# Optimization experiments

Hardware: AMD Instinct MI355X
Metric: run time of the kernel (lower is better)

The kernel has to match this reference:

```python
import jax, jax.numpy as jnp
import numpy as np

D_MODEL, D_STATE, D_CONV, EXPAND, L = 512, 16, 4, 2, 2048
D_INNER = EXPAND * D_MODEL


def _dwconv_causal(x, w, b):
    # x: (L, D), w: (D, K), b: (D,). torch Conv1d(groups=D, padding=K-1)[..., :L]
    K = w.shape[1]
    xp = jnp.pad(x, ((K - 1, 0), (0, 0)))
    windows = jnp.stack([xp[k:k + x.shape[0]] for k in range(K)], axis=-1)  # (L, D, K)
    return jnp.einsum('ldk,dk->ld', windows, w) + b


def _ssm_dir(x, inW, inb, cw, cb, xpW, xpb, dtW, dtb, outW, outb, A_log, Dp):
    xz = x @ inW + inb                      # (L, 2*Di)
    x_ssm, z = xz[:, :D_INNER], xz[:, D_INNER:]
    x_ssm = _dwconv_causal(x_ssm, cw, cb)   # (L, Di)
    sp = jax.nn.silu(x_ssm) @ xpW + xpb     # (L, Di + 2*S)
    delta = sp[:, :D_INNER]
    B = sp[:, D_INNER:D_INNER + D_STATE]
    C = sp[:, D_INNER + D_STATE:]
    dt = jax.nn.softplus(delta @ dtW + dtb)  # (L, Di)
    A = -jnp.exp(A_log)                      # (Di, S)
    dA = jnp.exp(dt[:, :, None] * A[None])                      # (L, Di, S)
    dBu = dt[:, :, None] * B[:, None, :] * x_ssm[:, :, None]    # (L, Di, S)

    def step(h, inp):
        a, bu = inp
        h = a * h + bu
        return h, h

    h0 = jnp.zeros((D_INNER, D_STATE), x.dtype)
    _, hs = jax.lax.scan(step, h0, (dA, dBu))   # (L, Di, S)
    y = jnp.einsum('lds,ls->ld', hs, C) + Dp * x_ssm
    return (y * jax.nn.silu(z)) @ outW + outb


def _make_params(key):
    ks = jax.random.split(key, 32)
    i = iter(range(32))
    def w(shape, scale=0.02):
        return (jax.random.normal(ks[next(i)], shape, jnp.float32) * scale)
    p = {}
    for pre in ('fwd_', 'bwd_'):
        p[pre + 'in_W'] = w((D_MODEL, 2 * D_INNER))
        p[pre + 'in_b'] = w((2 * D_INNER,))
        p[pre + 'conv_w'] = w((D_INNER, D_CONV), 0.1)
        p[pre + 'conv_b'] = w((D_INNER,))
        p[pre + 'xp_W'] = w((D_INNER, D_INNER + 2 * D_STATE))
        p[pre + 'xp_b'] = w((D_INNER + 2 * D_STATE,))
        p[pre + 'dt_W'] = w((D_INNER, D_INNER))
        p[pre + 'dt_b'] = w((D_INNER,))
        p[pre + 'out_W'] = w((D_INNER, D_MODEL))
        p[pre + 'out_b'] = w((D_MODEL,))
    p['A_log'] = jax.random.normal(ks[next(i)], (D_INNER, D_STATE), jnp.float32) * 0.5
    p['D_param'] = jnp.ones((D_INNER,), jnp.float32)
    p['fusion_W'] = w((2 * D_MODEL, D_MODEL))
    p['fusion_b'] = w((D_MODEL,))
    return p


def setup_inputs() -> dict:
    key = jax.random.key(0)
    kx, kp = jax.random.split(key)
    inp = {'x': jax.random.normal(kx, (L, D_MODEL), jnp.float32)}
    inp.update(_make_params(kp))
    return inp


def reference(x,
              fwd_in_W, fwd_in_b, fwd_conv_w, fwd_conv_b, fwd_xp_W, fwd_xp_b,
              fwd_dt_W, fwd_dt_b, fwd_out_W, fwd_out_b,
              bwd_in_W, bwd_in_b, bwd_conv_w, bwd_conv_b, bwd_xp_W, bwd_xp_b,
              bwd_dt_W, bwd_dt_b, bwd_out_W, bwd_out_b,
              A_log, D_param, fusion_W, fusion_b):
    out_fwd = _ssm_dir(x, fwd_in_W, fwd_in_b, fwd_conv_w, fwd_conv_b,
                       fwd_xp_W, fwd_xp_b, fwd_dt_W, fwd_dt_b,
                       fwd_out_W, fwd_out_b, A_log, D_param)
    out_bwd = _ssm_dir(x[::-1], bwd_in_W, bwd_in_b, bwd_conv_w, bwd_conv_b,
                       bwd_xp_W, bwd_xp_b, bwd_dt_W, bwd_dt_b,
                       bwd_out_W, bwd_out_b, A_log, D_param)[::-1]
    return jnp.concatenate([out_fwd, out_bwd], axis=-1) @ fusion_W + fusion_b
```

## Files before the change

### kernel.cpp

```cpp
#include <hip/hip_runtime.h>
#include <cmath>

#define L_SEQ 2048
#define DM 512
#define DI 1024
#define DS 16
#define NSP 1056
#define NC 64
#define CL 32

typedef unsigned short ushortT;
typedef unsigned int u32;
typedef __attribute__((ext_vector_type(8))) short short8;
typedef __attribute__((ext_vector_type(4))) float float4_t;
typedef __attribute__((address_space(1))) u32 gu32;
typedef __attribute__((address_space(3))) u32 lu32;

__device__ __forceinline__ float sigm(float x) { return 1.0f / (1.0f + __expf(-x)); }

__device__ __forceinline__ ushortT f2bf(float f) {
    unsigned u = __float_as_uint(f);
    unsigned r = u + 0x7FFFu + ((u >> 16) & 1u);
    return (ushortT)(r >> 16);
}

__device__ __forceinline__ void gl2lds16(const ushortT* g, ushortT* l) {
    __builtin_amdgcn_global_load_lds((gu32*)g, (lu32*)l, 16, 0, 0);
}

__global__ __launch_bounds__(256) void wcvt_k(const float* __restrict__ W,
                                              ushortT* __restrict__ Wt,
                                              int K, int N)
{
    __shared__ ushortT t[32][33];
    int n0 = blockIdx.x * 32, k0 = blockIdx.y * 32;
    int tx = threadIdx.x & 31, ty = threadIdx.x >> 5;
    #pragma unroll
    for (int i = 0; i < 32; i += 8)
        t[ty + i][tx] = f2bf(W[(size_t)(k0 + ty + i) * N + n0 + tx]);
    __syncthreads();
    #pragma unroll
    for (int i = 0; i < 32; i += 8)
        Wt[(size_t)(n0 + ty + i) * K + k0 + tx] = t[tx][ty + i];
}

__global__ __launch_bounds__(256) void xcvt_k(const float* __restrict__ x,
                                              ushortT* __restrict__ xb, int n)
{
    int i = (blockIdx.x * 256 + threadIdx.x) * 4;
    if (i < n) {
        float4_t v = *(const float4_t*)(x + i);
        xb[i + 0] = f2bf(v[0]); xb[i + 1] = f2bf(v[1]);
        xb[i + 2] = f2bf(v[2]); xb[i + 3] = f2bf(v[3]);
    }
}

template<int BM, int BN>
__global__ __launch_bounds__(256, 2) void gemm_bf16(
    const ushortT* __restrict__ A, int lda, long long Astr, int revAmode,
    const ushortT* __restrict__ W, long long Wstr,
    const float* __restrict__ bias0, const float* __restrict__ bias1,
    float* __restrict__ Cf, int ldcf, long long Cfstr,
    ushortT* __restrict__ Cb, int ldcb, long long Cbstr, int Nbmax,
    int revCmode, int M, int N, int K, int epi)
{
    const int dir = blockIdx.z;
    A  += (size_t)dir * Astr;
    W  += (size_t)dir * Wstr;
    if (Cf) Cf += (size_t)dir * Cfstr;
    if (Cb) Cb += (size_t)dir * Cbstr;
    const float* bias = dir ? bias1 : bias0;
    const int revA = (revAmode == 2) ? dir : revAmode;
    const int revC = (revCmode == 2) ? dir : revCmode;

    constexpr int MI = BM / 32;
    constexpr int NI = BN / 32;
    constexpr int CA = BM / 64;
    constexpr int CB = BN / 64;

    __shared__ ushortT As[BM * 32];
    __shared__ ushortT Bs[BN * 32];

    const int tid  = threadIdx.x;
    const int wave = tid >> 6;
    const int lane = tid & 63;
    const int quad = lane >> 4;
    const int r    = lane & 15;
    const int wm   = (wave >> 1) * (BM / 2);
    const int wn   = (wave & 1) * (BN / 2);
    const int bm   = blockIdx.y * BM;
    const int bn   = blockIdx.x * BN;

    const int lrow = lane >> 2;
    const int lk   = (lane & 3) * 8;

    const ushortT* gA[CA];
    ushortT* lA[CA];
    #pragma unroll
    for (int c = 0; c < CA; ++c) {
        int row = bm + c * 64 + wave * 16 + lrow;
        if (revA) row = M - 1 - row;
        gA[c] = A + (size_t)row * lda + lk;
        lA[c] = As + (c * 64 + wave * 16) * 32;
    }
    const ushortT* gB[CB];
    ushortT* lB[CB];
    #pragma unroll
    for (int c = 0; c < CB; ++c) {
        int row = bn + c * 64 + wave * 16 + lrow;
        if (row > N - 1) row = N - 1;
        gB[c] = W + (size_t)row * K + lk;
        lB[c] = Bs + (c * 64 + wave * 16) * 32;
    }

    float4_t acc[MI][NI];
    #pragma unroll
    for (int i = 0; i < MI; ++i)
        #pragma unroll
        for (int j = 0; j < NI; ++j)
            acc[i][j] = (float4_t){0.f, 0.f, 0.f, 0.f};

    for (int k0 = 0; k0 < K; k0 += 32) {
        #pragma unroll
        for (int c = 0; c < CA; ++c) gl2lds16(gA[c] + k0, lA[c]);
        #pragma unroll
        for (int c = 0; c < CB; ++c) gl2lds16(gB[c] + k0, lB[c]);
        __syncthreads();

        short8 af[MI], bf[NI];
        #pragma unroll
        for (int mi = 0; mi < MI; ++mi)
            af[mi] = *(const short8*)&As[(wm + mi * 16 + r) * 32 + quad * 8];
        #pragma unroll
        for (int ni = 0; ni < NI; ++ni)
            bf[ni] = *(const short8*)&Bs[(wn + ni * 16 + r) * 32 + quad * 8];
        #pragma unroll
        for (int mi = 0; mi < MI; ++mi)
            #pragma unroll
            for (int ni = 0; ni < NI; ++ni)
                acc[mi][ni] = __builtin_amdgcn_mfma_f32_16x16x32_bf16(
                    af[mi], bf[ni], acc[mi][ni], 0, 0, 0);
        __syncthreads();
    }

    #pragma unroll
    for (int mi = 0; mi < MI; ++mi) {
        int rowb = bm + wm + mi * 16 + quad * 4;
        #pragma unroll
        for (int ni = 0; ni < NI; ++ni) {
            int gn = bn + wn + ni * 16 + r;
            if (gn < N) {
                float bv = bias[gn];
                #pragma unroll
                for (int j = 0; j < 4; ++j) {
                    int orow = rowb + j;
                    if (revC) orow = M - 1 - orow;
                    float v = acc[mi][ni][j] + bv;
                    if (epi == 1) v = (v > 20.0f) ? v : log1pf(__expf(v));
                    if (Cf) Cf[(size_t)orow * ldcf + gn] = v;
                    if (Cb && gn < Nbmax) Cb[(size_t)orow * ldcb + gn] = f2bf(v);
                }
            }
        }
    }
}

__global__ __launch_bounds__(256) void conv_k(
    const float* __restrict__ XZ, const float* __restrict__ cw,
    const float* __restrict__ cb, float* __restrict__ XC, ushortT* __restrict__ SCb)
{
    int idx = blockIdx.x * 256 + threadIdx.x;
    int d = idx & (DI - 1);
    int l = idx >> 10;
    float w0 = cw[d * 4 + 0], w1 = cw[d * 4 + 1], w2 = cw[d * 4 + 2], w3 = cw[d * 4 + 3];
    float acc = cb[d];
    if (l >= 3) acc += XZ[(size_t)(l - 3) * (2 * DI) + d] * w0;
    if (l >= 2) acc += XZ[(size_t)(l - 2) * (2 * DI) + d] * w1;
    if (l >= 1) acc += XZ[(size_t)(l - 1) * (2 * DI) + d] * w2;
    acc += XZ[(size_t)l * (2 * DI) + d] * w3;
    XC[idx] = acc;
    SCb[idx] = f2bf(acc * sigm(acc));
}

__global__ __launch_bounds__(256) void scanA_k(
    const float* __restrict__ DT, const float* __restrict__ XC,
    const float* __restrict__ SP, const float* __restrict__ Alog,
    float* __restrict__ Pend, float* __restrict__ Hl)
{
    __shared__ float Bsh[CL][DS];
    int dir = blockIdx.z;
    int c = blockIdx.y;
    int d = blockIdx.x * 256 + threadIdx.x;
    DT += (size_t)dir * L_SEQ * DI;
    XC += (size_t)dir * L_SEQ * DI;
    SP += (size_t)dir * L_SEQ * NSP;
    int l0 = c * CL;
    for (int i = threadIdx.x; i < CL * DS; i += 256) {
        int ll = i >> 4, ss = i & 15;
        Bsh[ll][ss] = SP[(size_t)(l0 + ll) * NSP + DI + ss];
    }
    __syncthreads();
    float Ae[DS], h[DS], P[DS];
    #pragma unroll
    for (int s = 0; s < DS; ++s) { Ae[s] = -__expf(Alog[d * DS + s]); h[s] = 0.f; P[s] = 1.f; }
    for (int t = 0; t < CL; ++t) {
        int l = l0 + t;
        float dt = DT[(size_t)l * DI + d];
        float xv = XC[(size_t)l * DI + d];
        float dtx = dt * xv;
        #pragma unroll
        for (int s = 0; s < DS; ++s) {
            float e = __expf(dt * Ae[s]);
            h[s] = e * h[s] + dtx * Bsh[t][s];
            P[s] *= e;
        }
    }
    size_t o = ((size_t)(dir * NC + c) * DI + d) * DS;
    #pragma unroll
    for (int s = 0; s < DS; ++s) { Pend[o + s] = P[s]; Hl[o + s] = h[s]; }
}

__global__ __launch_bounds__(256) void scanB_k(
    const float* __restrict__ Pend, const float* __restrict__ Hl, float* __restrict__ Hs)
{
    int idx = blockIdx.x * 256 + threadIdx.x;
    float h = 0.f;
    int ds = idx & 16383;
    int dir = idx >> 14;
    for (int c = 0; c < NC; ++c) {
        size_t o = ((size_t)(dir * NC + c)) * (DI * DS) + ds;
        Hs[o] = h;
        h = Pend[o] * h + Hl[o];
    }
}

__global__ __launch_bounds__(256) void scanC_k(
    const float* __restrict__ DT, const float* __restrict__ XC,
    const float* __restrict__ SP, const float* __restrict__ XZ,
    const float* __restrict__ Alog, const float* __restrict__ Dp,
    const float* __restrict__ Hs, ushortT* __restrict__ Gb)
{
    __shared__ float Bsh[CL][DS];
    __shared__ float Csh[CL][DS];
    int dir = blockIdx.z;
    int c = blockIdx.y;
    int d = blockIdx.x * 256 + threadIdx.x;
    DT += (size_t)dir * L_SEQ * DI;
    XC += (size_t)dir * L_SEQ * DI;
    SP += (size_t)dir * L_SEQ * NSP;
    XZ += (size_t)dir * L_SEQ * (2 * DI);
    Gb += (size_t)dir * L_SEQ * DI;
    int l0 = c * CL;
    for (int i = threadIdx.x; i < CL * DS; i += 256) {
        int ll = i >> 4, ss = i & 15;
        size_t base = (size_t)(l0 + ll) * NSP + DI;
        Bsh[ll][ss] = SP[base + ss];
        Csh[ll][ss] = SP[base + DS + ss];
    }
    __syncthreads();
    float Ae[DS], h[DS];
    size_t o = ((size_t)(dir * NC + c) * DI + d) * DS;
    #pragma unroll
    for (int s = 0; s < DS; ++s) { Ae[s] = -__expf(Alog[d * DS + s]); h[s] = Hs[o + s]; }
    float dpv = Dp[d];
    for (int t = 0; t < CL; ++t) {
        int l = l0 + t;
        float dt = DT[(size_t)l * DI + d];
        float xv = XC[(size_t)l * DI + d];
        float dtx = dt * xv;
        float y = 0.f;
        #pragma unroll
        for (int s = 0; s < DS; ++s) {
            float e = __expf(dt * Ae[s]);
            h[s] = e * h[s] + dtx * Bsh[t][s];
            y += h[s] * Csh[t][s];
        }
        y += dpv * xv;
        float z = XZ[(size_t)l * (2 * DI) + DI + d];
        Gb[(size_t)l * DI + d] = f2bf(y * (z * sigm(z)));
    }
}

extern "C" void kernel_launch(void* const* d_in, const int* in_sizes, int n_in,
                              void* d_out, int out_size, void* d_ws, size_t ws_size,
                              hipStream_t stream)
{
    (void)in_sizes; (void)n_in; (void)out_size; (void)ws_size;
    const float* x = (const float*)d_in[0];
    const float* inW[2]  = {(const float*)d_in[1],  (const float*)d_in[11]};
    const float* inb[2]  = {(const float*)d_in[2],  (const float*)d_in[12]};
    const float* cw[2]   = {(const float*)d_in[3],  (const float*)d_in[13]};
    const float* cb[2]   = {(const float*)d_in[4],  (const float*)d_in[14]};
    const float* xpW[2]  = {(const float*)d_in[5],  (const float*)d_in[15]};
    const float* xpb[2]  = {(const float*)d_in[6],  (const float*)d_in[16]};
    const float* dtW[2]  = {(const float*)d_in[7],  (const float*)d_in[17]};
    const float* dtb[2]  = {(const float*)d_in[8],  (const float*)d_in[18]};
    const float* outW[2] = {(const float*)d_in[9],  (const float*)d_in[19]};
    const float* outb[2] = {(const float*)d_in[10], (const float*)d_in[20]};
    const float* Alog = (const float*)d_in[21];
    const float* Dp   = (const float*)d_in[22];
    const float* fuW  = (const float*)d_in[23];
    const float* fub  = (const float*)d_in[24];
    float* out = (float*)d_out;

    float* ws = (float*)d_ws;
    size_t off = 0;
    auto alloc = [&](size_t n) { float* p = ws + off; off += n; return p; };
    float* XZ  = alloc((size_t)2 * L_SEQ * 2 * DI);
    float* XC  = alloc((size_t)2 * L_SEQ * DI);
    float* SP  = alloc((size_t)2 * L_SEQ * NSP);
    float* DTb = alloc((size_t)2 * L_SEQ * DI);
    float* Pend= alloc((size_t)2 * NC * DI * DS);
    float* Hl  = alloc((size_t)2 * NC * DI * DS);
    float* Hs  = alloc((size_t)2 * NC * DI * DS);

    ushortT* wsu = (ushortT*)(ws + off);
    size_t uoff = 0;
    auto ualloc = [&](size_t n) { ushortT* p = wsu + uoff; uoff += n; return p; };
    ushortT* WtIn  = ualloc((size_t)2 * (2 * DI) * DM);
    ushortT* WtXp  = ualloc((size_t)2 * NSP * DI);
    ushortT* WtDt  = ualloc((size_t)2 * DI * DI);
    ushortT* WtOut = ualloc((size_t)2 * DM * DI);
    ushortT* WtFu  = ualloc((size_t)DM * DI);
    ushortT* XB    = ualloc((size_t)L_SEQ * DM);
    ushortT* SCb   = ualloc((size_t)2 * L_SEQ * DI);
    ushortT* SPb   = ualloc((size_t)2 * L_SEQ * DI);
    ushortT* Gb    = ualloc((size_t)2 * L_SEQ * DI);
    ushortT* OCb   = ualloc((size_t)L_SEQ * DI);

    dim3 blk(256);
    for (int dir = 0; dir < 2; ++dir) {
        wcvt_k<<<dim3(2 * DI / 32, DM / 32), blk, 0, stream>>>(inW[dir],  WtIn  + (size_t)dir * 2 * DI * DM, DM, 2 * DI);
        wcvt_k<<<dim3(NSP / 32,   DI / 32),  blk, 0, stream>>>(xpW[dir],  WtXp  + (size_t)dir * NSP * DI,    DI, NSP);
        wcvt_k<<<dim3(DI / 32,    DI / 32),  blk, 0, stream>>>(dtW[dir],  WtDt  + (size_t)dir * DI * DI,     DI, DI);
        wcvt_k<<<dim3(DM / 32,    DI / 32),  blk, 0, stream>>>(outW[dir], WtOut + (size_t)dir * DM * DI,     DI, DM);
    }
    wcvt_k<<<dim3(DM / 32, DI / 32), blk, 0, stream>>>(fuW, WtFu, DI, DM);
    xcvt_k<<<dim3(L_SEQ * DM / 1024), blk, 0, stream>>>(x, XB, L_SEQ * DM);

    gemm_bf16<128, 128><<<dim3(16, 16, 2), blk, 0, stream>>>(
        XB, DM, 0, 2, WtIn, (long long)2 * DI * DM, inb[0], inb[1],
        XZ, 2 * DI, (long long)L_SEQ * 2 * DI, nullptr, 0, 0, 0,
        0, L_SEQ, 2 * DI, DM, 0);
    for (int dir = 0; dir < 2; ++dir)
        conv_k<<<dim3(L_SEQ * DI / 256), blk, 0, stream>>>(
            XZ + (size_t)dir * L_SEQ * 2 * DI, cw[dir], cb[dir],
            XC + (size_t)dir * L_SEQ * DI, SCb + (size_t)dir * L_SEQ * DI);
    gemm_bf16<128, 64><<<dim3((NSP + 63) / 64, 16, 2), blk, 0, stream>>>(
        SCb, DI, (long long)L_SEQ * DI, 0, WtXp, (long long)NSP * DI, xpb[0], xpb[1],
        SP, NSP, (long long)L_SEQ * NSP, SPb, DI, (long long)L_SEQ * DI, DI,
        0, L_SEQ, NSP, DI, 0);
    gemm_bf16<128, 64><<<dim3(16, 16, 2), blk, 0, stream>>>(
        SPb, DI, (long long)L_SEQ * DI, 0, WtDt, (long long)DI * DI, dtb[0], dtb[1],
        DTb, DI, (long long)L_SEQ * DI, nullptr, 0, 0, 0,
        0, L_SEQ, DI, DI, 1);
    scanA_k<<<dim3(DI / 256, NC, 2), blk, 0, stream>>>(DTb, XC, SP, Alog, Pend, Hl);
    scanB_k<<<dim3(2 * DI * DS / 256), blk, 0, stream>>>(Pend, Hl, Hs);
    scanC_k<<<dim3(DI / 256, NC, 2), blk, 0, stream>>>(DTb, XC, SP, XZ, Alog, Dp, Hs, Gb);
    gemm_bf16<64, 64><<<dim3(8, 32, 2), blk, 0, stream>>>(
        Gb, DI, (long long)L_SEQ * DI, 0, WtOut, (long long)DM * DI, outb[0], outb[1],
        nullptr, 0, 0, OCb, DI, (long long)DM, DM,
        2, L_SEQ, DM, DI, 0);
    gemm_bf16<64, 64><<<dim3(8, 32, 1), blk, 0, stream>>>(
        OCb, DI, 0, 0, WtFu, 0, fub, fub,
        out, DM, (long long)0, nullptr, 0, 0, 0,
        0, L_SEQ, DM, DI, 0);
}
```

Baseline: 363.5 us.

## Double-buffer GEMM LDS tiles and batch weight-convert and conv launches

The bf16 MFMA GEMM now keeps two LDS buffers, so the direct-to-LDS global load for the next K slice is issued before the MFMAs on the current slice. This lets memory latency overlap with compute. Separately, the nine weight-conversion launches are merged into one kernel that looks up its matrix from a block-offset table, and the two per-direction conv launches become one launch with a z dimension, cutting launch overhead. The GEMM's LDS use doubles, which may lower occupancy. The two-step unrolled loop assumes an even number of K steps, which holds for the K values used here.

```diff
diff --git a/kernel.cpp b/kernel.cpp
--- a/kernel.cpp
+++ b/kernel.cpp
@@ -28,12 +28,25 @@
     __builtin_amdgcn_global_load_lds((gu32*)g, (lu32*)l, 16, 0, 0);
 }
 
-__global__ __launch_bounds__(256) void wcvt_k(const float* __restrict__ W,
-                                              ushortT* __restrict__ Wt,
-                                              int K, int N)
+struct WC {
+    const float* src[9];
+    ushortT* dst[9];
+    int K[9], N[9], tN[9];
+    int off[10];
+};
+
+__global__ __launch_bounds__(256) void wcvt_all(WC wc)
 {
     __shared__ ushortT t[32][33];
-    int n0 = blockIdx.x * 32, k0 = blockIdx.y * 32;
+    int b = blockIdx.x;
+    int m = 0;
+    while (b >= wc.off[m + 1]) ++m;
+    int tl = b - wc.off[m];
+    int n0 = (tl % wc.tN[m]) * 32;
+    int k0 = (tl / wc.tN[m]) * 32;
+    const float* W = wc.src[m];
+    ushortT* Wt = wc.dst[m];
+    int K = wc.K[m], N = wc.N[m];
     int tx = threadIdx.x & 31, ty = threadIdx.x >> 5;
     #pragma unroll
     for (int i = 0; i < 32; i += 8)
@@ -78,8 +91,8 @@
     constexpr int CA = BM / 64;
     constexpr int CB = BN / 64;
 
-    __shared__ ushortT As[BM * 32];
-    __shared__ ushortT Bs[BN * 32];
+    __shared__ ushortT As[2][BM * 32];
+    __shared__ ushortT Bs[2][BN * 32];
 
     const int tid  = threadIdx.x;
     const int wave = tid >> 6;
@@ -101,7 +114,7 @@
         int row = bm + c * 64 + wave * 16 + lrow;
         if (revA) row = M - 1 - row;
         gA[c] = A + (size_t)row * lda + lk;
-        lA[c] = As + (c * 64 + wave * 16) * 32;
+        lA[c] = &As[0][(c * 64 + wave * 16) * 32];
     }
     const ushortT* gB[CB];
     ushortT* lB[CB];
@@ -110,8 +123,10 @@
         int row = bn + c * 64 + wave * 16 + lrow;
         if (row > N - 1) row = N - 1;
         gB[c] = W + (size_t)row * K + lk;
-        lB[c] = Bs + (c * 64 + wave * 16) * 32;
-    }
+        lB[c] = &Bs[0][(c * 64 + wave * 16) * 32];
+    }
+    constexpr int ABUF = BM * 32;
+    constexpr int BBUF = BN * 32;
 
     float4_t acc[MI][NI];
     #pragma unroll
@@ -120,27 +135,64 @@
         for (int j = 0; j < NI; ++j)
             acc[i][j] = (float4_t){0.f, 0.f, 0.f, 0.f};
 
-    for (int k0 = 0; k0 < K; k0 += 32) {
-        #pragma unroll
-        for (int c = 0; c < CA; ++c) gl2lds16(gA[c] + k0, lA[c]);
-        #pragma unroll
-        for (int c = 0; c < CB; ++c) gl2lds16(gB[c] + k0, lB[c]);
+    const int nsteps = K >> 5;
+
+    #pragma unroll
+    for (int c = 0; c < CA; ++c) gl2lds16(gA[c], lA[c]);
+    #pragma unroll
+    for (int c = 0; c < CB; ++c) gl2lds16(gB[c], lB[c]);
+
+    for (int i = 0; i < nsteps; i += 2) {
         __syncthreads();
-
-        short8 af[MI], bf[NI];
-        #pragma unroll
-        for (int mi = 0; mi < MI; ++mi)
-            af[mi] = *(const short8*)&As[(wm + mi * 16 + r) * 32 + quad * 8];
-        #pragma unroll
-        for (int ni = 0; ni < NI; ++ni)
-            bf[ni] = *(const short8*)&Bs[(wn + ni * 16 + r) * 32 + quad * 8];
-        #pragma unroll
-        for (int mi = 0; mi < MI; ++mi)
+        {
+            int kq = (i + 1) << 5;
+            if (i + 1 < nsteps) {
+                #pragma unroll
+                for (int c = 0; c < CA; ++c) gl2lds16(gA[c] + kq, lA[c] + ABUF);
+                #pragma unroll
+                for (int c = 0; c < CB; ++c) gl2lds16(gB[c] + kq, lB[c] + BBUF);
+            }
+        }
+        {
+            short8 af[MI], bf[NI];
+            #pragma unroll
+            for (int mi = 0; mi < MI; ++mi)
+                af[mi] = *(const short8*)&As[0][(wm + mi * 16 + r) * 32 + quad * 8];
             #pragma unroll
             for (int ni = 0; ni < NI; ++ni)
-                acc[mi][ni] = __builtin_amdgcn_mfma_f32_16x16x32_bf16(
-                    af[mi], bf[ni], acc[mi][ni], 0, 0, 0);
+                bf[ni] = *(const short8*)&Bs[0][(wn + ni * 16 + r) * 32 + quad * 8];
+            #pragma unroll
+            for (int mi = 0; mi < MI; ++mi)
+                #pragma unroll
+                for (int ni = 0; ni < NI; ++ni)
+                    acc[mi][ni] = __builtin_amdgcn_mfma_f32_16x16x32_bf16(
+                        af[mi], bf[ni], acc[mi][ni], 0, 0, 0);
+        }
         __syncthreads();
+        {
+            int kq = (i + 2) << 5;
+            if (i + 2 < nsteps) {
+                #pragma unroll
+                for (int c = 0; c < CA; ++c) gl2lds16(gA[c] + kq, lA[c]);
+                #pragma unroll
+                for (int c = 0; c < CB; ++c) gl2lds16(gB[c] + kq, lB[c]);
+            }
+        }
+        {
+            short8 af[MI], bf[NI];
+            #pragma unroll
+            for (int mi = 0; mi < MI; ++mi)
+                af[mi] = *(const short8*)&As[1][(wm + mi * 16 + r) * 32 + quad * 8];
+            #pragma unroll
+            for (int ni = 0; ni < NI; ++ni)
+                bf[ni] = *(const short8*)&Bs[1][(wn + ni * 16 + r) * 32 + quad * 8];
+            #pragma unroll
+            for (int mi = 0; mi < MI; ++mi)
+                #pragma unroll
+                for (int ni = 0; ni < NI; ++ni)
+                    acc[mi][ni] = __builtin_amdgcn_mfma_f32_16x16x32_bf16(
+                        af[mi], bf[ni], acc[mi][ni], 0, 0, 0);
+        }
     }
 
     #pragma unroll
@@ -166,9 +218,17 @@
 }
 
 __global__ __launch_bounds__(256) void conv_k(
-    const float* __restrict__ XZ, const float* __restrict__ cw,
-    const float* __restrict__ cb, float* __restrict__ XC, ushortT* __restrict__ SCb)
-{
+    const float* __restrict__ XZ,
+    const float* __restrict__ cw0, const float* __restrict__ cw1,
+    const float* __restrict__ cb0, const float* __restrict__ cb1,
+    float* __restrict__ XC, ushortT* __restrict__ SCb)
+{
+    int dir = blockIdx.z;
+    XZ += (size_t)dir * L_SEQ * 2 * DI;
+    XC += (size_t)dir * L_SEQ * DI;
+    SCb += (size_t)dir * L_SEQ * DI;
+    const float* cw = dir ? cw1 : cw0;
+    const float* cb = dir ? cb1 : cb0;
     int idx = blockIdx.x * 256 + threadIdx.x;
     int d = idx & (DI - 1);
     int l = idx >> 10;
@@ -329,23 +389,33 @@
     ushortT* OCb   = ualloc((size_t)L_SEQ * DI);
 
     dim3 blk(256);
-    for (int dir = 0; dir < 2; ++dir) {
-        wcvt_k<<<dim3(2 * DI / 32, DM / 32), blk, 0, stream>>>(inW[dir],  WtIn  + (size_t)dir * 2 * DI * DM, DM, 2 * DI);
-        wcvt_k<<<dim3(NSP / 32,   DI / 32),  blk, 0, stream>>>(xpW[dir],  WtXp  + (size_t)dir * NSP * DI,    DI, NSP);
-        wcvt_k<<<dim3(DI / 32,    DI / 32),  blk, 0, stream>>>(dtW[dir],  WtDt  + (size_t)dir * DI * DI,     DI, DI);
-        wcvt_k<<<dim3(DM / 32,    DI / 32),  blk, 0, stream>>>(outW[dir], WtOut + (size_t)dir * DM * DI,     DI, DM);
-    }
-    wcvt_k<<<dim3(DM / 32, DI / 32), blk, 0, stream>>>(fuW, WtFu, DI, DM);
+
+    WC wc;
+    const float* srcs[9] = {inW[0], inW[1], xpW[0], xpW[1], dtW[0], dtW[1],
+                            outW[0], outW[1], fuW};
+    ushortT* dsts[9] = {WtIn, WtIn + (size_t)2 * DI * DM,
+                        WtXp, WtXp + (size_t)NSP * DI,
+                        WtDt, WtDt + (size_t)DI * DI,
+                        WtOut, WtOut + (size_t)DM * DI,
+                        WtFu};
+    int Ks[9] = {DM, DM, DI, DI, DI, DI, DI, DI, DI};
+    int Ns[9] = {2 * DI, 2 * DI, NSP, NSP, DI, DI, DM, DM, DM};
+    wc.off[0] = 0;
+    for (int m = 0; m < 9; ++m) {
+        wc.src[m] = srcs[m]; wc.dst[m] = dsts[m];
+        wc.K[m] = Ks[m]; wc.N[m] = Ns[m];
+        wc.tN[m] = Ns[m] / 32;
+        wc.off[m + 1] = wc.off[m] + (Ns[m] / 32) * (Ks[m] / 32);
+    }
+    wcvt_all<<<dim3(wc.off[9]), blk, 0, stream>>>(wc);
     xcvt_k<<<dim3(L_SEQ * DM / 1024), blk, 0, stream>>>(x, XB, L_SEQ * DM);
 
     gemm_bf16<128, 128><<<dim3(16, 16, 2), blk, 0, stream>>>(
         XB, DM, 0, 2, WtIn, (long long)2 * DI * DM, inb[0], inb[1],
         XZ, 2 * DI, (long long)L_SEQ * 2 * DI, nullptr, 0, 0, 0,
         0, L_SEQ, 2 * DI, DM, 0);
-    for (int dir = 0; dir < 2; ++dir)
-        conv_k<<<dim3(L_SEQ * DI / 256), blk, 0, stream>>>(
-            XZ + (size_t)dir * L_SEQ * 2 * DI, cw[dir], cb[dir],
-            XC + (size_t)dir * L_SEQ * DI, SCb + (size_t)dir * L_SEQ * DI);
+    conv_k<<<dim3(L_SEQ * DI / 256, 1, 2), blk, 0, stream>>>(
+        XZ, cw[0], cw[1], cb[0], cb[1], XC, SCb);
     gemm_bf16<128, 64><<<dim3((NSP + 63) / 64, 16, 2), blk, 0, stream>>>(
         SCb, DI, (long long)L_SEQ * DI, 0, WtXp, (long long)NSP * DI, xpb[0], xpb[1],
         SP, NSP, (long long)L_SEQ * NSP, SPb, DI, (long long)L_SEQ * DI, DI,
```

After: 346.8 us. -4.6%, faster.
